# Kernel optimization log

Measured on AMD Instinct MI355X. Metric: run time of the kernel, lower is better.

## Reference

```python
import jax, jax.numpy as jnp
import numpy as np

IMG = 28      # image side
WS = 2        # window (patch) side
NPS = IMG // WS          # patches per side = 14
NP = NPS * NPS           # 196 patches
NW = 12                  # circuit weights: 4+2+4+2
NC = 10                  # classes
B = 512                  # batch

_CX = jnp.array([[1, 0, 0, 0],
                 [0, 1, 0, 0],
                 [0, 0, 0, 1],
                 [0, 0, 1, 0]], dtype=jnp.complex64)  # basis |control,target>


def _ry(theta):
    # RY(theta) = [[cos(t/2), -sin(t/2)], [sin(t/2), cos(t/2)]]; theta scalar or (M,)
    c = jnp.cos(theta * 0.5)
    s = jnp.sin(theta * 0.5)
    return jnp.stack([jnp.stack([c, -s], -1),
                      jnp.stack([s, c], -1)], -2).astype(jnp.complex64)


def _crx(theta):
    # controlled-RX, 4x4 in |control,target> basis (identity on control=0 block)
    c = jnp.cos(theta * 0.5).astype(jnp.complex64)
    s = jnp.sin(theta * 0.5).astype(jnp.complex64)
    U = jnp.eye(4, dtype=jnp.complex64)
    U = U.at[2, 2].set(c).at[3, 3].set(c)
    U = U.at[2, 3].set(-1j * s).at[3, 2].set(-1j * s)
    return U


def _ap1(st, U, q):
    # apply 1-qubit gate U (2,2) or per-sample (M,2,2) on qubit q; st: (M,2,2,2,2)
    st = jnp.moveaxis(st, 1 + q, 4)
    if U.ndim == 2:
        st = jnp.einsum('ij,mabcj->mabci', U, st)
    else:
        st = jnp.einsum('mij,mabcj->mabci', U, st)
    return jnp.moveaxis(st, 4, 1 + q)


def _ap2(st, U, qc, qt):
    # apply 2-qubit gate U (4,4) with control qc, target qt
    st = jnp.moveaxis(st, (1 + qc, 1 + qt), (3, 4))
    M = st.shape[0]
    st = jnp.einsum('ij,mabj->mabi', U, st.reshape(M, 2, 2, 4)).reshape(M, 2, 2, 2, 2)
    return jnp.moveaxis(st, (3, 4), (1 + qc, 1 + qt))


def _qcnn(angles, qw):
    # angles: (M,4) input rotation angles; qw: (12,) shared circuit weights
    # returns (M,3) Bloch vector [<X>,<Y>,<Z>] of qubit 0
    M = angles.shape[0]
    st = jnp.zeros((M, 2, 2, 2, 2), jnp.complex64).at[:, 0, 0, 0, 0].set(1.0)
    for q in range(4):                       # data encoding
        st = _ap1(st, _ry(angles[:, q]), q)
    # conv1
    st = _ap1(st, _ry(qw[0]), 0)
    st = _ap1(st, _ry(qw[1]), 1)
    st = _ap2(st, _CX, 0, 1)
    st = _ap1(st, _ry(qw[2]), 2)
    st = _ap1(st, _ry(qw[3]), 3)
    st = _ap2(st, _CX, 2, 3)
    st = _ap2(st, _CX, 1, 2)
    st = _ap2(st, _CX, 3, 0)
    # pool1
    st = _ap2(st, _crx(qw[4]), 1, 0)
    st = _ap2(st, _crx(qw[5]), 3, 2)
    # conv2
    st = _ap1(st, _ry(qw[6]), 0)
    st = _ap1(st, _ry(qw[7]), 2)
    st = _ap2(st, _CX, 0, 2)
    st = _ap1(st, _ry(qw[8]), 0)
    st = _ap1(st, _ry(qw[9]), 2)
    # pool2
    st = _ap2(st, _crx(qw[10]), 2, 0)
    st = _ap1(st, _ry(qw[11]), 0)
    # expectations on qubit 0 via reduced density matrix entries
    a = jnp.moveaxis(st, 1, 4).reshape(M, 8, 2)       # (M, other-qubits, qubit0)
    r01 = jnp.sum(a[:, :, 0] * jnp.conj(a[:, :, 1]), axis=1)
    ex = 2.0 * jnp.real(r01)
    ey = -2.0 * jnp.imag(r01)
    p0 = jnp.sum(jnp.real(a[:, :, 0] * jnp.conj(a[:, :, 0])), axis=1)
    p1 = jnp.sum(jnp.real(a[:, :, 1] * jnp.conj(a[:, :, 1])), axis=1)
    return jnp.stack([ex, ey, p0 - p1], -1)


def setup_inputs() -> dict:
    key = jax.random.key(0)
    k1, k2, k3 = jax.random.split(key, 3)
    x = jax.random.uniform(k1, (B, 1, IMG, IMG), jnp.float32)         # pixel values in [0,1]
    qw = jax.random.uniform(k2, (NW,), jnp.float32, -1.0, 1.0)         # circuit weights
    fc_w = jax.random.normal(k3, (NC, NP * 3), jnp.float32) * 0.02
    fc_b = jnp.zeros((NC,), jnp.float32)
    return {"x": x, "qw": qw, "fc_w": fc_w, "fc_b": fc_b}


def reference(x, qw, fc_w, fc_b):
    b = x.shape[0]
    img = x.reshape(b, IMG, IMG)
    # 2x2 stride-2 patches, row-major within patch (matches torch unfold+view)
    p = img.reshape(b, NPS, WS, NPS, WS).transpose(0, 1, 3, 2, 4).reshape(b, NP, WS * WS)
    angles = (p * jnp.pi).reshape(b * NP, 4)
    feats = _qcnn(angles, qw).reshape(b, NP * 3)      # (B, 588)
    return feats @ fc_w.T + fc_b                      # (B, 10)
```

## Files before the change

### kernel.cpp

```cpp
#include <hip/hip_runtime.h>
#include <math.h>

#define IMGS 28
#define NPSD 14
#define NPAT 196
#define NCLS 10
#define NFEAT (NPAT * 3)

__device__ __forceinline__ void fsincos(float x, float& s, float& c) {
    s = __sinf(x);
    c = __cosf(x);
}


template <int MASK>
__device__ __forceinline__ void ry_gate(float (&sr)[16], float (&si)[16], float c, float s) {
#pragma unroll
    for (int i = 0; i < 16; ++i) {
        if (i & MASK) continue;
        const int j = i | MASK;
        float r0 = sr[i], q0 = si[i], r1 = sr[j], q1 = si[j];
        sr[i] = c * r0 - s * r1;  si[i] = c * q0 - s * q1;
        sr[j] = s * r0 + c * r1;  si[j] = s * q0 + c * q1;
    }
}

template <int MC, int MT>
__device__ __forceinline__ void cx_gate(float (&sr)[16], float (&si)[16]) {
#pragma unroll
    for (int i = 0; i < 16; ++i) {
        if ((i & MC) && !(i & MT)) {
            const int j = i | MT;
            float tr = sr[i], ti = si[i];
            sr[i] = sr[j]; si[i] = si[j];
            sr[j] = tr;    si[j] = ti;
        }
    }
}

template <int MC, int MT>
__device__ __forceinline__ void crx_gate(float (&sr)[16], float (&si)[16], float c, float s) {
#pragma unroll
    for (int i = 0; i < 16; ++i) {
        if ((i & MC) && !(i & MT)) {
            const int j = i | MT;
            float r0 = sr[i], q0 = si[i], r1 = sr[j], q1 = si[j];
            sr[i] = c * r0 + s * q1;  si[i] = c * q0 - s * r1;
            sr[j] = c * r1 + s * q0;  si[j] = c * q1 - s * r0;
        }
    }
}

__global__ __launch_bounds__(256) void qcnn_fused_kernel(
        const float* __restrict__ x, const float* __restrict__ qw,
        const float* __restrict__ fc_w, const float* __restrict__ fc_b,
        float* __restrict__ out) {
    __shared__ float feats[NFEAT];

    const int b = blockIdx.x;
    const int t = threadIdx.x;

    if (t < NPAT) {
        const int pr = t / NPSD, pc = t % NPSD;
        const float* img = x + (size_t)b * (IMGS * IMGS);
        const float* p0 = img + (2 * pr) * IMGS + 2 * pc;
        const float a0 = p0[0], a1 = p0[1], a2 = p0[IMGS], a3 = p0[IMGS + 1];

        float ce[4], se[4];
        const float HPI = 1.57079632679489662f;
        fsincos(a0 * HPI, se[0], ce[0]);
        fsincos(a1 * HPI, se[1], ce[1]);
        fsincos(a2 * HPI, se[2], ce[2]);
        fsincos(a3 * HPI, se[3], ce[3]);

        float sr[16], si[16];
#pragma unroll
        for (int i = 0; i < 16; ++i) {
            float v = ((i & 8) ? se[0] : ce[0]) * ((i & 4) ? se[1] : ce[1]) *
                      ((i & 2) ? se[2] : ce[2]) * ((i & 1) ? se[3] : ce[3]);
            sr[i] = v;
            si[i] = 0.0f;
        }

        float cw[12], sw[12];
#pragma unroll
        for (int i = 0; i < 12; ++i) fsincos(qw[i] * 0.5f, sw[i], cw[i]);

        ry_gate<8>(sr, si, cw[0], sw[0]);
        ry_gate<4>(sr, si, cw[1], sw[1]);
        cx_gate<8, 4>(sr, si);
        ry_gate<2>(sr, si, cw[2], sw[2]);
        ry_gate<1>(sr, si, cw[3], sw[3]);
        cx_gate<2, 1>(sr, si);
        cx_gate<4, 2>(sr, si);
        cx_gate<1, 8>(sr, si);
        crx_gate<4, 8>(sr, si, cw[4], sw[4]);
        crx_gate<1, 2>(sr, si, cw[5], sw[5]);
        ry_gate<8>(sr, si, cw[6], sw[6]);
        ry_gate<2>(sr, si, cw[7], sw[7]);
        cx_gate<8, 2>(sr, si);
        ry_gate<8>(sr, si, cw[8], sw[8]);
        ry_gate<2>(sr, si, cw[9], sw[9]);
        crx_gate<2, 8>(sr, si, cw[10], sw[10]);
        ry_gate<8>(sr, si, cw[11], sw[11]);

        float ex = 0.f, ey = 0.f, ez = 0.f;
#pragma unroll
        for (int j = 0; j < 8; ++j) {
            float r0 = sr[j], q0 = si[j], r1 = sr[j + 8], q1 = si[j + 8];
            ex += r0 * r1 + q0 * q1;
            ey += r0 * q1 - q0 * r1;
            ez += (r0 * r0 + q0 * q0) - (r1 * r1 + q1 * q1);
        }
        feats[t * 3 + 0] = 2.0f * ex;
        feats[t * 3 + 1] = 2.0f * ey;
        feats[t * 3 + 2] = ez;
    }

    __syncthreads();

    if (t < NCLS * 16) {
        const int c = t >> 4, l = t & 15;
        const float* w = fc_w + c * NFEAT;
        float acc = 0.0f;
        for (int j = l; j < NFEAT; j += 16) acc += feats[j] * w[j];
#pragma unroll
        for (int off = 8; off >= 1; off >>= 1) acc += __shfl_xor(acc, off, 64);
        if (l == 0) out[b * NCLS + c] = acc + fc_b[c];
    }
}

extern "C" void kernel_launch(void* const* d_in, const int* in_sizes, int n_in,
                              void* d_out, int out_size, void* d_ws, size_t ws_size,
                              hipStream_t stream) {
    const float* x    = (const float*)d_in[0];
    const float* qw   = (const float*)d_in[1];
    const float* fc_w = (const float*)d_in[2];
    const float* fc_b = (const float*)d_in[3];
    float* out = (float*)d_out;

    const int B = in_sizes[0] / (IMGS * IMGS);
    qcnn_fused_kernel<<<B, 256, 0, stream>>>(x, qw, fc_w, fc_b, out);
}
```

Before: 12.56 us.

## Fold FC layer into per-patch threads with wave-level shuffle reduction

Each patch thread now multiplies its three Bloch features directly by the matching fc_w entries for all ten classes. The per-class sums are reduced across each 64-lane wave with xor shuffles, and the four wave partials are combined through a small shared array. This drops the shared feature buffer and the serial strided dot-product phase that ran after the barrier. In exchange it adds ten six-step shuffle reductions per wave and uncoalesced stride-3 loads of fc_w.

Result: faster. 10.16 us (-19.1%).

```diff
diff --git a/kernel.cpp b/kernel.cpp
--- a/kernel.cpp
+++ b/kernel.cpp
@@ -55,10 +55,14 @@
         const float* __restrict__ x, const float* __restrict__ qw,
         const float* __restrict__ fc_w, const float* __restrict__ fc_b,
         float* __restrict__ out) {
-    __shared__ float feats[NFEAT];
+    __shared__ float partial[4][NCLS];
 
     const int b = blockIdx.x;
     const int t = threadIdx.x;
+
+    float con[NCLS];
+#pragma unroll
+    for (int c = 0; c < NCLS; ++c) con[c] = 0.0f;
 
     if (t < NPAT) {
         const int pr = t / NPSD, pc = t % NPSD;
@@ -112,21 +116,34 @@
             ey += r0 * q1 - q0 * r1;
             ez += (r0 * r0 + q0 * q0) - (r1 * r1 + q1 * q1);
         }
-        feats[t * 3 + 0] = 2.0f * ex;
-        feats[t * 3 + 1] = 2.0f * ey;
-        feats[t * 3 + 2] = ez;
+        ex *= 2.0f;
+        ey *= 2.0f;
+
+#pragma unroll
+        for (int c = 0; c < NCLS; ++c) {
+            const float* w = fc_w + c * NFEAT + 3 * t;
+            con[c] = ex * w[0] + ey * w[1] + ez * w[2];
+        }
     }
 
+#pragma unroll
+    for (int c = 0; c < NCLS; ++c) {
+        float v = con[c];
+#pragma unroll
+        for (int off = 32; off >= 1; off >>= 1) v += __shfl_xor(v, off, 64);
+        con[c] = v;
+    }
+
+    const int wave = t >> 6, lane = t & 63;
+    if (lane == 0) {
+#pragma unroll
+        for (int c = 0; c < NCLS; ++c) partial[wave][c] = con[c];
+    }
     __syncthreads();
 
-    if (t < NCLS * 16) {
-        const int c = t >> 4, l = t & 15;
-        const float* w = fc_w + c * NFEAT;
-        float acc = 0.0f;
-        for (int j = l; j < NFEAT; j += 16) acc += feats[j] * w[j];
-#pragma unroll
-        for (int off = 8; off >= 1; off >>= 1) acc += __shfl_xor(acc, off, 64);
-        if (l == 0) out[b * NCLS + c] = acc + fc_b[c];
+    if (t < NCLS) {
+        out[b * NCLS + t] = partial[0][t] + partial[1][t] + partial[2][t] +
+                            partial[3][t] + fc_b[t];
     }
 }
 
```
